# Performance work log

Measured on AMD Instinct MI355X. Metric: run time of the kernel, lower is better.

## Reference

```python
import jax, jax.numpy as jnp
import numpy as np

HEADS = 8
DIM_HEAD = 64
ROPE_THETA = 10000.0


def _rope(t):
    # t: [b, h, n, d]; interleaved-pair rotation as in rotary-embedding-torch
    n, d = t.shape[-2], t.shape[-1]
    inv_freq = 1.0 / (ROPE_THETA ** (jnp.arange(0, d, 2, dtype=jnp.float32) / d))  # [d/2]
    freqs = jnp.arange(n, dtype=jnp.float32)[:, None] * inv_freq[None, :]  # [n, d/2]
    freqs = jnp.repeat(freqs, 2, axis=-1)  # [n, d], repeated per pair
    cos, sin = jnp.cos(freqs), jnp.sin(freqs)
    x1 = t[..., 0::2]
    x2 = t[..., 1::2]
    rot = jnp.stack((-x2, x1), axis=-1).reshape(t.shape)  # rotate_half
    return t * cos + rot * sin


def setup_inputs() -> dict:
    key = jax.random.key(0)
    k1, k2, k3, k4 = jax.random.split(key, 4)
    b, n, dim = 2, 2048, 512
    hidden = HEADS * DIM_HEAD
    x = jax.random.normal(k1, (b, n, dim), dtype=jnp.float32)
    pos_bias = jax.random.normal(k2, (HEADS, n, n), dtype=jnp.float32) * 0.02
    w_qkv = jax.random.normal(k3, (dim, 3 * hidden), dtype=jnp.float32) * (dim ** -0.5)
    w_out = jax.random.normal(k4, (hidden, dim), dtype=jnp.float32) * (hidden ** -0.5)
    return {"x": x, "pos_bias": pos_bias, "w_qkv": w_qkv, "w_out": w_out}


def reference(x, pos_bias, w_qkv, w_out):
    b, n, _ = x.shape
    qkv = x @ w_qkv  # [b, n, 3*hidden]
    q, k, v = jnp.split(qkv, 3, axis=-1)

    def to_heads(t):
        return t.reshape(b, n, HEADS, DIM_HEAD).transpose(0, 2, 1, 3)  # [b,h,n,d]

    q, k, v = map(to_heads, (q, k, v))
    k = _rope(k)
    q = _rope(q * (DIM_HEAD ** -0.5))
    sim = jnp.einsum('bhid,bhjd->bhij', q, k)  # [b,h,n,n]
    sim = sim + pos_bias  # broadcast over batch
    sim = sim - jax.lax.stop_gradient(jnp.max(sim, axis=-1, keepdims=True))
    attn = jax.nn.softmax(sim, axis=-1)
    out = jnp.einsum('bhij,bhjd->bhid', attn, v)
    out = out.transpose(0, 2, 1, 3).reshape(b, n, HEADS * DIM_HEAD)
    return out @ w_out
```

## Files before the change

kernel.cpp:

```cpp
#include <hip/hip_runtime.h>
#include <math.h>

#define SEQ 2048
#define NHEAD 8
#define HDIM 64
#define BATCH 2
#define MTOT 4096

typedef __attribute__((ext_vector_type(8))) short short8;
typedef __attribute__((ext_vector_type(4))) float f32x4;

__device__ __forceinline__ ushort f2bf(float f) {
    union { float f; unsigned u; } v; v.f = f;
    unsigned r = v.u + 0x7FFFu + ((v.u >> 16) & 1u);
    return (ushort)(r >> 16);
}

__device__ __forceinline__ f32x4 mfma16(short8 a, short8 b, f32x4 c) {
    return __builtin_amdgcn_mfma_f32_16x16x32_bf16(a, b, c, 0, 0, 0);
}

__global__ __launch_bounds__(256)
void pack_x(const float* __restrict__ x, ushort* __restrict__ xb)
{
    const int i = (blockIdx.x * 256 + threadIdx.x) * 8;
    float4 a = *(const float4*)&x[i];
    float4 b = *(const float4*)&x[i + 4];
    union { ushort us[8]; uint4 v; } pk;
    pk.us[0] = f2bf(a.x); pk.us[1] = f2bf(a.y); pk.us[2] = f2bf(a.z); pk.us[3] = f2bf(a.w);
    pk.us[4] = f2bf(b.x); pk.us[5] = f2bf(b.y); pk.us[6] = f2bf(b.z); pk.us[7] = f2bf(b.w);
    *(uint4*)&xb[i] = pk.v;
}

__global__ __launch_bounds__(256)
void transpose_w(const float* __restrict__ w, ushort* __restrict__ wT, int K, int N)
{
    __shared__ ushort tile[64][66];
    const int t = threadIdx.x;
    const int n0 = blockIdx.x * 64, k0 = blockIdx.y * 64;
#pragma unroll
    for (int i = 0; i < 4; ++i) {
        const int slot = t + i * 256;
        const int r = slot >> 4, c4 = (slot & 15) * 4;
        float4 v = *(const float4*)&w[(size_t)(k0 + r) * N + n0 + c4];
        tile[c4 + 0][r] = f2bf(v.x);
        tile[c4 + 1][r] = f2bf(v.y);
        tile[c4 + 2][r] = f2bf(v.z);
        tile[c4 + 3][r] = f2bf(v.w);
    }
    __syncthreads();
    const int n = t >> 2, kc = (t & 3) * 16;
    union { ushort us[16]; uint4 v[2]; } o;
#pragma unroll
    for (int j = 0; j < 16; ++j) o.us[j] = tile[n][kc + j];
    *(uint4*)&wT[(size_t)(n0 + n) * K + k0 + kc]     = o.v[0];
    *(uint4*)&wT[(size_t)(n0 + n) * K + k0 + kc + 8] = o.v[1];
}

__global__ __launch_bounds__(256)
void gemm_qkv_rope(const ushort* __restrict__ xb, const ushort* __restrict__ wT,
                   ushort* __restrict__ qb, ushort* __restrict__ kb,
                   ushort* __restrict__ vb)
{
    __shared__ __align__(16) ushort As[128][72];
    __shared__ __align__(16) ushort Bs[128][72];
    const int t = threadIdx.x, lane = t & 63, w = t >> 6;
    const int quad = lane >> 4, l16 = lane & 15;
    const int m0 = blockIdx.y * 128, n0 = blockIdx.x * 128;
    const int mw = (w >> 1) * 64, nw = (w & 1) * 64;
    f32x4 acc[4][4] = {};

    for (int k0 = 0; k0 < 512; k0 += 64) {
#pragma unroll
        for (int i = 0; i < 4; ++i) {
            const int slot = t + i * 256;
            const int r = slot >> 3, sg = (slot & 7) * 8;
            *(uint4*)&As[r][sg] = *(const uint4*)&xb[(size_t)(m0 + r) * 512 + k0 + sg];
            *(uint4*)&Bs[r][sg] = *(const uint4*)&wT[(size_t)(n0 + r) * 512 + k0 + sg];
        }
        __syncthreads();
#pragma unroll
        for (int ks = 0; ks < 2; ++ks) {
            short8 a[4], b[4];
#pragma unroll
            for (int i = 0; i < 4; ++i)
                a[i] = *(const short8*)&As[mw + i * 16 + l16][ks * 32 + quad * 8];
#pragma unroll
            for (int j = 0; j < 4; ++j)
                b[j] = *(const short8*)&Bs[nw + j * 16 + l16][ks * 32 + quad * 8];
#pragma unroll
            for (int i = 0; i < 4; ++i)
#pragma unroll
                for (int j = 0; j < 4; ++j)
                    acc[i][j] = mfma16(a[i], b[j], acc[i][j]);
        }
        __syncthreads();
    }

    const int sec = (n0 + nw) >> 9;
#pragma unroll
    for (int i = 0; i < 4; ++i)
#pragma unroll
    for (int r = 0; r < 4; ++r) {
        const int m = m0 + mw + i * 16 + quad * 4 + r;
        const int bidx = m >> 11, n = m & 2047;
#pragma unroll
        for (int j = 0; j < 4; ++j) {
            const int nc = n0 + nw + j * 16 + l16;
            const int d = nc & 63, h = (nc >> 6) & 7;
            float vacc = acc[i][j][r];
            float outv; ushort* dst;
            if (sec == 2) { outv = vacc; dst = vb; }
            else {
                const int jj = d >> 1;
                const float inv = __expf(-(float)(2 * jj) * (9.2103403719761836f / 64.0f));
                float sn, cs; sincosf((float)n * inv, &sn, &cs);
                const float partner = __shfl_xor(vacc, 1);
                float rot = (d & 1) ? (vacc * cs + partner * sn)
                                    : (vacc * cs - partner * sn);
                if (sec == 0) { outv = rot * 0.125f; dst = qb; }
                else          { outv = rot;          dst = kb; }
            }
            dst[(((size_t)bidx * 8 + h) * 2048 + n) * 64 + d] = f2bf(outv);
        }
    }
}

__global__ __launch_bounds__(256)
void flash_attn_mfma(const ushort* __restrict__ qb, const ushort* __restrict__ kb,
                     const ushort* __restrict__ vb, const float* __restrict__ bias,
                     ushort* __restrict__ ob)
{
    __shared__ __align__(16) ushort Ks[64][72];
    __shared__ __align__(16) ushort Vt[64][72];
    __shared__ __align__(16) ushort Ps[4][16][72];
    const int t = threadIdx.x, lane = t & 63, w = t >> 6;
    const int quad = lane >> 4, l16 = lane & 15;
    const int q0 = blockIdx.x * 64, h = blockIdx.y, b = blockIdx.z;
    const size_t bh = (size_t)(b * NHEAD + h);
    const ushort* Q = qb + bh * SEQ * HDIM;
    const ushort* K = kb + bh * SEQ * HDIM;
    const ushort* V = vb + bh * SEQ * HDIM;

    short8 qf[2];
    qf[0] = *(const short8*)&Q[(size_t)(q0 + w * 16 + l16) * HDIM + quad * 8];
    qf[1] = *(const short8*)&Q[(size_t)(q0 + w * 16 + l16) * HDIM + 32 + quad * 8];

    f32x4 oacc[4] = {};
    float mrow[4] = {-1e30f, -1e30f, -1e30f, -1e30f};
    float lrow[4] = {};
    const float* bias_base = bias + ((size_t)h * SEQ + q0 + w * 16 + quad * 4) * SEQ;

    for (int k0 = 0; k0 < SEQ; k0 += 64) {
#pragma unroll
        for (int i = 0; i < 2; ++i) {
            const int slot = t + i * 256;
            const int r = slot >> 3, sg = (slot & 7) * 8;
            *(uint4*)&Ks[r][sg] = *(const uint4*)&K[(size_t)(k0 + r) * HDIM + sg];
        }
#pragma unroll
        for (int i = 0; i < 2; ++i) {
            const int slot = t + i * 256;
            const int c = slot & 63, rb = ((slot >> 6) & 7) * 8;
            union { ushort us[8]; uint4 v; } pk;
#pragma unroll
            for (int j = 0; j < 8; ++j)
                pk.us[j] = V[(size_t)(k0 + rb + j) * HDIM + c];
            *(uint4*)&Vt[c][rb] = pk.v;
        }
        __syncthreads();

        float bv[4][4];
#pragma unroll
        for (int r = 0; r < 4; ++r)
#pragma unroll
            for (int s = 0; s < 4; ++s)
                bv[r][s] = bias_base[(size_t)r * SEQ + k0 + s * 16 + l16];

        f32x4 sacc[4] = {};
#pragma unroll
        for (int ks = 0; ks < 2; ++ks)
#pragma unroll
            for (int s = 0; s < 4; ++s) {
                short8 kf = *(const short8*)&Ks[s * 16 + l16][ks * 32 + quad * 8];
                sacc[s] = mfma16(qf[ks], kf, sacc[s]);
            }

#pragma unroll
        for (int r = 0; r < 4; ++r) {
            float rm = -1e30f;
#pragma unroll
            for (int s = 0; s < 4; ++s) {
                sacc[s][r] += bv[r][s];
                rm = fmaxf(rm, sacc[s][r]);
            }
            rm = fmaxf(rm, __shfl_xor(rm, 1, 16));
            rm = fmaxf(rm, __shfl_xor(rm, 2, 16));
            rm = fmaxf(rm, __shfl_xor(rm, 4, 16));
            rm = fmaxf(rm, __shfl_xor(rm, 8, 16));
            const float mnew  = fmaxf(mrow[r], rm);
            const float alpha = __expf(mrow[r] - mnew);
            mrow[r] = mnew;
            float rs = 0.0f;
#pragma unroll
            for (int s = 0; s < 4; ++s) {
                const float p = __expf(sacc[s][r] - mnew);
                sacc[s][r] = p;
                rs += p;
            }
            rs += __shfl_xor(rs, 1, 16);
            rs += __shfl_xor(rs, 2, 16);
            rs += __shfl_xor(rs, 4, 16);
            rs += __shfl_xor(rs, 8, 16);
            lrow[r] = lrow[r] * alpha + rs;
#pragma unroll
            for (int s = 0; s < 4; ++s) oacc[s][r] *= alpha;
        }

#pragma unroll
        for (int r = 0; r < 4; ++r)
#pragma unroll
            for (int s = 0; s < 4; ++s)
                Ps[w][quad * 4 + r][s * 16 + l16] = f2bf(sacc[s][r]);
        asm volatile("" ::: "memory");

#pragma unroll
        for (int ks = 0; ks < 2; ++ks) {
            short8 pf = *(const short8*)&Ps[w][l16][ks * 32 + quad * 8];
#pragma unroll
            for (int s = 0; s < 4; ++s) {
                short8 vf = *(const short8*)&Vt[s * 16 + l16][ks * 32 + quad * 8];
                oacc[s] = mfma16(pf, vf, oacc[s]);
            }
        }
        __syncthreads();
    }

#pragma unroll
    for (int r = 0; r < 4; ++r) {
        const float invl = 1.0f / lrow[r];
        const size_t m = (size_t)b * SEQ + q0 + w * 16 + quad * 4 + r;
#pragma unroll
        for (int s = 0; s < 4; ++s)
            ob[m * 512 + h * HDIM + s * 16 + l16] = f2bf(oacc[s][r] * invl);
    }
}

__global__ __launch_bounds__(256)
void gemm_out(const ushort* __restrict__ Ab, const ushort* __restrict__ wT,
              float* __restrict__ C)
{
    __shared__ __align__(16) ushort As[64][72];
    __shared__ __align__(16) ushort Bs[128][72];
    const int t = threadIdx.x, lane = t & 63, w = t >> 6;
    const int quad = lane >> 4, l16 = lane & 15;
    const int m0 = blockIdx.y * 64, n0 = blockIdx.x * 128;
    const int mw = (w >> 1) * 32, nw = (w & 1) * 64;
    f32x4 acc[2][4] = {};

    for (int k0 = 0; k0 < 512; k0 += 64) {
#pragma unroll
        for (int i = 0; i < 2; ++i) {
            const int slot = t + i * 256;
            const int r = slot >> 3, sg = (slot & 7) * 8;
            *(uint4*)&As[r][sg] = *(const uint4*)&Ab[(size_t)(m0 + r) * 512 + k0 + sg];
        }
#pragma unroll
        for (int i = 0; i < 4; ++i) {
            const int slot = t + i * 256;
            const int r = slot >> 3, sg = (slot & 7) * 8;
            *(uint4*)&Bs[r][sg] = *(const uint4*)&wT[(size_t)(n0 + r) * 512 + k0 + sg];
        }
        __syncthreads();
#pragma unroll
        for (int ks = 0; ks < 2; ++ks) {
            short8 a[2], b[4];
#pragma unroll
            for (int i = 0; i < 2; ++i)
                a[i] = *(const short8*)&As[mw + i * 16 + l16][ks * 32 + quad * 8];
#pragma unroll
            for (int j = 0; j < 4; ++j)
                b[j] = *(const short8*)&Bs[nw + j * 16 + l16][ks * 32 + quad * 8];
#pragma unroll
            for (int i = 0; i < 2; ++i)
#pragma unroll
                for (int j = 0; j < 4; ++j)
                    acc[i][j] = mfma16(a[i], b[j], acc[i][j]);
        }
        __syncthreads();
    }
#pragma unroll
    for (int i = 0; i < 2; ++i)
#pragma unroll
    for (int r = 0; r < 4; ++r) {
        const int m = m0 + mw + i * 16 + quad * 4 + r;
#pragma unroll
        for (int j = 0; j < 4; ++j)
            C[(size_t)m * 512 + n0 + nw + j * 16 + l16] = acc[i][j][r];
    }
}

extern "C" void kernel_launch(void* const* d_in, const int* in_sizes, int n_in,
                              void* d_out, int out_size, void* d_ws, size_t ws_size,
                              hipStream_t stream)
{
    const float* x        = (const float*)d_in[0];
    const float* pos_bias = (const float*)d_in[1];
    const float* w_qkv    = (const float*)d_in[2];
    const float* w_out    = (const float*)d_in[3];
    float* out = (float*)d_out;

    char* ws = (char*)d_ws;
    ushort* xb     = (ushort*)(ws);
    ushort* wqkvT  = (ushort*)(ws + 4194304);
    ushort* woutT  = (ushort*)(ws + 5767168);
    ushort* qb     = (ushort*)(ws + 6291456);
    ushort* kb     = (ushort*)(ws + 10485760);
    ushort* vb     = (ushort*)(ws + 14680064);
    ushort* attnb  = (ushort*)(ws + 18874368);

    pack_x<<<1024, 256, 0, stream>>>(x, xb);
    transpose_w<<<dim3(24, 8), 256, 0, stream>>>(w_qkv, wqkvT, 512, 1536);
    transpose_w<<<dim3(8, 8), 256, 0, stream>>>(w_out, woutT, 512, 512);
    gemm_qkv_rope<<<dim3(12, 32), 256, 0, stream>>>(xb, wqkvT, qb, kb, vb);
    flash_attn_mfma<<<dim3(SEQ / 64, NHEAD, BATCH), 256, 0, stream>>>(qb, kb, vb, pos_bias, attnb);
    gemm_out<<<dim3(4, 64), 256, 0, stream>>>(attnb, woutT, out);
}
```

Measured before the change: 290.8 us.

## Drop online-softmax rescaling, store V pre-transposed, and use fast sincos in rope

The attention loop no longer tracks a running row max or rescales the accumulators. It exponentiates score plus bias directly, accumulates per-lane partial sums, and reduces them once at the end. The QKV GEMM epilogue now writes V in a [b,h,d,n] transposed layout, so attention loads V tiles with vector copies instead of a strided scalar gather. The rope epilogue hoists the inverse frequency, uses __sincosf, and the bias loads are issued before the K/V tile loads. Skipping max subtraction is mathematically equivalent, but exp can overflow if logits are large; it only stays safe because the scores here are small.

```diff
diff --git a/kernel.cpp b/kernel.cpp
--- a/kernel.cpp
+++ b/kernel.cpp
@@ -5,7 +5,6 @@
 #define NHEAD 8
 #define HDIM 64
 #define BATCH 2
-#define MTOT 4096
 
 typedef __attribute__((ext_vector_type(8))) short short8;
 typedef __attribute__((ext_vector_type(4))) float f32x4;
@@ -60,7 +59,7 @@
 __global__ __launch_bounds__(256)
 void gemm_qkv_rope(const ushort* __restrict__ xb, const ushort* __restrict__ wT,
                    ushort* __restrict__ qb, ushort* __restrict__ kb,
-                   ushort* __restrict__ vb)
+                   ushort* __restrict__ vtb)
 {
     __shared__ __align__(16) ushort As[128][72];
     __shared__ __align__(16) ushort Bs[128][72];
@@ -98,37 +97,50 @@
     }
 
     const int sec = (n0 + nw) >> 9;
-#pragma unroll
-    for (int i = 0; i < 4; ++i)
-#pragma unroll
-    for (int r = 0; r < 4; ++r) {
-        const int m = m0 + mw + i * 16 + quad * 4 + r;
-        const int bidx = m >> 11, n = m & 2047;
+    if (sec == 2) {
+#pragma unroll
+        for (int i = 0; i < 4; ++i) {
+            const int m = m0 + mw + i * 16 + quad * 4;
+            const int bidx = m >> 11, n = m & 2047;
+#pragma unroll
+            for (int j = 0; j < 4; ++j) {
+                const int nc = n0 + nw + j * 16 + l16;
+                const int d = nc & 63, h = (nc >> 6) & 7;
+                ushort4 pk;
+                pk.x = f2bf(acc[i][j][0]); pk.y = f2bf(acc[i][j][1]);
+                pk.z = f2bf(acc[i][j][2]); pk.w = f2bf(acc[i][j][3]);
+                *(ushort4*)&vtb[(((size_t)bidx * 8 + h) * 64 + d) * 2048 + n] = pk;
+            }
+        }
+    } else {
+        ushort* dst = (sec == 0) ? qb : kb;
+        const float scale = (sec == 0) ? 0.125f : 1.0f;
 #pragma unroll
         for (int j = 0; j < 4; ++j) {
             const int nc = n0 + nw + j * 16 + l16;
             const int d = nc & 63, h = (nc >> 6) & 7;
-            float vacc = acc[i][j][r];
-            float outv; ushort* dst;
-            if (sec == 2) { outv = vacc; dst = vb; }
-            else {
-                const int jj = d >> 1;
-                const float inv = __expf(-(float)(2 * jj) * (9.2103403719761836f / 64.0f));
-                float sn, cs; sincosf((float)n * inv, &sn, &cs);
+            const float inv = __expf(-(float)(d & ~1) * (9.2103403719761836f / 64.0f));
+#pragma unroll
+            for (int i = 0; i < 4; ++i)
+#pragma unroll
+            for (int r = 0; r < 4; ++r) {
+                const int m = m0 + mw + i * 16 + quad * 4 + r;
+                const int bidx = m >> 11, n = m & 2047;
+                float sn, cs;
+                __sincosf((float)n * inv, &sn, &cs);
+                const float vacc = acc[i][j][r];
                 const float partner = __shfl_xor(vacc, 1);
-                float rot = (d & 1) ? (vacc * cs + partner * sn)
-                                    : (vacc * cs - partner * sn);
-                if (sec == 0) { outv = rot * 0.125f; dst = qb; }
-                else          { outv = rot;          dst = kb; }
-            }
-            dst[(((size_t)bidx * 8 + h) * 2048 + n) * 64 + d] = f2bf(outv);
+                const float rot = (d & 1) ? (vacc * cs + partner * sn)
+                                          : (vacc * cs - partner * sn);
+                dst[(((size_t)bidx * 8 + h) * 2048 + n) * 64 + d] = f2bf(rot * scale);
+            }
         }
     }
 }
 
 __global__ __launch_bounds__(256)
 void flash_attn_mfma(const ushort* __restrict__ qb, const ushort* __restrict__ kb,
-                     const ushort* __restrict__ vb, const float* __restrict__ bias,
+                     const ushort* __restrict__ vtb, const float* __restrict__ bias,
                      ushort* __restrict__ ob)
 {
     __shared__ __align__(16) ushort Ks[64][72];
@@ -138,44 +150,34 @@
     const int quad = lane >> 4, l16 = lane & 15;
     const int q0 = blockIdx.x * 64, h = blockIdx.y, b = blockIdx.z;
     const size_t bh = (size_t)(b * NHEAD + h);
-    const ushort* Q = qb + bh * SEQ * HDIM;
-    const ushort* K = kb + bh * SEQ * HDIM;
-    const ushort* V = vb + bh * SEQ * HDIM;
+    const ushort* Q  = qb  + bh * SEQ * HDIM;
+    const ushort* K  = kb  + bh * SEQ * HDIM;
+    const ushort* VT = vtb + bh * HDIM * SEQ;
 
     short8 qf[2];
     qf[0] = *(const short8*)&Q[(size_t)(q0 + w * 16 + l16) * HDIM + quad * 8];
     qf[1] = *(const short8*)&Q[(size_t)(q0 + w * 16 + l16) * HDIM + 32 + quad * 8];
 
     f32x4 oacc[4] = {};
-    float mrow[4] = {-1e30f, -1e30f, -1e30f, -1e30f};
-    float lrow[4] = {};
+    float lsum[4] = {};
     const float* bias_base = bias + ((size_t)h * SEQ + q0 + w * 16 + quad * 4) * SEQ;
 
     for (int k0 = 0; k0 < SEQ; k0 += 64) {
+        float bv[4][4];
+#pragma unroll
+        for (int r = 0; r < 4; ++r)
+#pragma unroll
+            for (int s = 0; s < 4; ++s)
+                bv[r][s] = bias_base[(size_t)r * SEQ + k0 + s * 16 + l16];
+
 #pragma unroll
         for (int i = 0; i < 2; ++i) {
             const int slot = t + i * 256;
             const int r = slot >> 3, sg = (slot & 7) * 8;
             *(uint4*)&Ks[r][sg] = *(const uint4*)&K[(size_t)(k0 + r) * HDIM + sg];
-        }
-#pragma unroll
-        for (int i = 0; i < 2; ++i) {
-            const int slot = t + i * 256;
-            const int c = slot & 63, rb = ((slot >> 6) & 7) * 8;
-            union { ushort us[8]; uint4 v; } pk;
-#pragma unroll
-            for (int j = 0; j < 8; ++j)
-                pk.us[j] = V[(size_t)(k0 + rb + j) * HDIM + c];
-            *(uint4*)&Vt[c][rb] = pk.v;
-        }
-        __syncthreads();
-
-        float bv[4][4];
-#pragma unroll
-        for (int r = 0; r < 4; ++r)
-#pragma unroll
-            for (int s = 0; s < 4; ++s)
-                bv[r][s] = bias_base[(size_t)r * SEQ + k0 + s * 16 + l16];
+            *(uint4*)&Vt[r][sg] = *(const uint4*)&VT[(size_t)r * SEQ + k0 + sg];
+        }
+        __syncthreads();
 
         f32x4 sacc[4] = {};
 #pragma unroll
@@ -188,40 +190,13 @@
 
 #pragma unroll
         for (int r = 0; r < 4; ++r) {
-            float rm = -1e30f;
 #pragma unroll
             for (int s = 0; s < 4; ++s) {
-                sacc[s][r] += bv[r][s];
-                rm = fmaxf(rm, sacc[s][r]);
-            }
-            rm = fmaxf(rm, __shfl_xor(rm, 1, 16));
-            rm = fmaxf(rm, __shfl_xor(rm, 2, 16));
-            rm = fmaxf(rm, __shfl_xor(rm, 4, 16));
-            rm = fmaxf(rm, __shfl_xor(rm, 8, 16));
-            const float mnew  = fmaxf(mrow[r], rm);
-            const float alpha = __expf(mrow[r] - mnew);
-            mrow[r] = mnew;
-            float rs = 0.0f;
-#pragma unroll
-            for (int s = 0; s < 4; ++s) {
-                const float p = __expf(sacc[s][r] - mnew);
-                sacc[s][r] = p;
-                rs += p;
-            }
-            rs += __shfl_xor(rs, 1, 16);
-            rs += __shfl_xor(rs, 2, 16);
-            rs += __shfl_xor(rs, 4, 16);
-            rs += __shfl_xor(rs, 8, 16);
-            lrow[r] = lrow[r] * alpha + rs;
-#pragma unroll
-            for (int s = 0; s < 4; ++s) oacc[s][r] *= alpha;
-        }
-
-#pragma unroll
-        for (int r = 0; r < 4; ++r)
-#pragma unroll
-            for (int s = 0; s < 4; ++s)
-                Ps[w][quad * 4 + r][s * 16 + l16] = f2bf(sacc[s][r]);
+                const float p = __expf(sacc[s][r] + bv[r][s]);
+                lsum[r] += p;
+                Ps[w][quad * 4 + r][s * 16 + l16] = f2bf(p);
+            }
+        }
         asm volatile("" ::: "memory");
 
 #pragma unroll
@@ -238,7 +213,12 @@
 
 #pragma unroll
     for (int r = 0; r < 4; ++r) {
-        const float invl = 1.0f / lrow[r];
+        float rs = lsum[r];
+        rs += __shfl_xor(rs, 1, 16);
+        rs += __shfl_xor(rs, 2, 16);
+        rs += __shfl_xor(rs, 4, 16);
+        rs += __shfl_xor(rs, 8, 16);
+        const float invl = 1.0f / rs;
         const size_t m = (size_t)b * SEQ + q0 + w * 16 + quad * 4 + r;
 #pragma unroll
         for (int s = 0; s < 4; ++s)
@@ -316,13 +296,13 @@
     ushort* woutT  = (ushort*)(ws + 5767168);
     ushort* qb     = (ushort*)(ws + 6291456);
     ushort* kb     = (ushort*)(ws + 10485760);
-    ushort* vb     = (ushort*)(ws + 14680064);
+    ushort* vtb    = (ushort*)(ws + 14680064);
     ushort* attnb  = (ushort*)(ws + 18874368);
 
     pack_x<<<1024, 256, 0, stream>>>(x, xb);
     transpose_w<<<dim3(24, 8), 256, 0, stream>>>(w_qkv, wqkvT, 512, 1536);
     transpose_w<<<dim3(8, 8), 256, 0, stream>>>(w_out, woutT, 512, 512);
-    gemm_qkv_rope<<<dim3(12, 32), 256, 0, stream>>>(xb, wqkvT, qb, kb, vb);
-    flash_attn_mfma<<<dim3(SEQ / 64, NHEAD, BATCH), 256, 0, stream>>>(qb, kb, vb, pos_bias, attnb);
+    gemm_qkv_rope<<<dim3(12, 32), 256, 0, stream>>>(xb, wqkvT, qb, kb, vtb);
+    flash_attn_mfma<<<dim3(SEQ / 64, NHEAD, BATCH), 256, 0, stream>>>(qb, kb, vtb, pos_bias, attnb);
     gemm_out<<<dim3(4, 64), 256, 0, stream>>>(attnb, woutT, out);
 }
```

Measured after the change: 285.3 us. Within noise of the previous version (-1.9%).
